# Optimization experiments

Hardware: AMD Instinct MI355X
Metric: run time of the kernel (lower is better)

The kernel has to match this reference:

```python
import jax, jax.numpy as jnp
from jax import lax
import numpy as np

B, L, F = 4, 1024, 32
DM, NL, DS, DC, EX, NH = 256, 4, 16, 4, 2, 4
DI = EX * DM            # 512 inner channels
DTR = (DM + 15) // 16   # dt_rank = 16


def setup_inputs() -> dict:
    key = jax.random.key(0)
    ks = jax.random.split(key, 12)
    s = 0.02
    rn = lambda k, shape: jax.random.normal(k, shape, jnp.float32) * s
    return dict(
        x=jax.random.normal(ks[0], (B, L, F), jnp.float32),
        proj_w=rn(ks[1], (DM, F)), proj_b=jnp.zeros((DM,), jnp.float32),
        inproj_w=rn(ks[2], (NL, 2 * DI, DM)),
        conv_w=rn(ks[3], (NL, DI, DC)), conv_b=jnp.zeros((NL, DI), jnp.float32),
        xproj_w=rn(ks[4], (NL, DTR + 2 * DS, DI)),
        dtproj_w=rn(ks[5], (NL, DI, DTR)), dtproj_b=rn(ks[6], (NL, DI)),
        A_log=jnp.tile(jnp.log(jnp.arange(1, DS + 1, dtype=jnp.float32))[None, None, :], (NL, DI, 1)),
        Dp=jnp.ones((NL, DI), jnp.float32),
        outproj_w=rn(ks[7], (NL, DM, DI)),
        ln_g=jnp.ones((NL, DM), jnp.float32), ln_b=jnp.zeros((NL, DM), jnp.float32),
        head_w1=rn(ks[8], (DM, DM)), head_b1=jnp.zeros((DM,), jnp.float32),
        head_w2=rn(ks[9], (NH, DM)), head_b2=jnp.zeros((NH,), jnp.float32),
    )


def _layernorm(x, g, b, eps=1e-5):
    mu = x.mean(axis=-1, keepdims=True)
    var = ((x - mu) ** 2).mean(axis=-1, keepdims=True)
    return (x - mu) * lax.rsqrt(var + eps) * g + b


def _mamba(x, inw, cw, cb, xpw, dtw, dtb, A_log, Dp, outw):
    b, l, _ = x.shape
    xz = x @ inw.T                       # (b,l,2*DI)
    u, z = xz[..., :DI], xz[..., DI:]
    # causal depthwise conv1d, kernel DC
    up = jnp.pad(u, ((0, 0), (DC - 1, 0), (0, 0)))
    uc = sum(up[:, k:k + l, :] * cw[:, k] for k in range(DC)) + cb
    uc = jax.nn.silu(uc)
    dbc = uc @ xpw.T                     # (b,l,DTR+2*DS)
    dt, Bc, Cc = dbc[..., :DTR], dbc[..., DTR:DTR + DS], dbc[..., DTR + DS:]
    delta = jax.nn.softplus(dt @ dtw.T + dtb)   # (b,l,DI)
    A = -jnp.exp(A_log)                  # (DI,DS)

    def step(h, inp):
        d_t, B_t, C_t, u_t = inp         # (b,DI),(b,DS),(b,DS),(b,DI)
        h = jnp.exp(d_t[..., None] * A) * h + (d_t * u_t)[..., None] * B_t[:, None, :]
        return h, jnp.einsum('bdn,bn->bd', h, C_t)

    h0 = jnp.zeros((b, DI, DS), x.dtype)
    xs = tuple(jnp.swapaxes(a, 0, 1) for a in (delta, Bc, Cc, uc))
    _, ys = lax.scan(step, h0, xs)       # ys: (l,b,DI)
    y = jnp.swapaxes(ys, 0, 1) + uc * Dp
    return (y * jax.nn.silu(z)) @ outw.T


def reference(x, proj_w, proj_b, inproj_w, conv_w, conv_b, xproj_w, dtproj_w, dtproj_b,
              A_log, Dp, outproj_w, ln_g, ln_b, head_w1, head_b1, head_w2, head_b2):
    h = x @ proj_w.T + proj_b
    for i in range(NL):
        blk = _mamba(h, inproj_w[i], conv_w[i], conv_b[i], xproj_w[i],
                     dtproj_w[i], dtproj_b[i], A_log[i], Dp[i], outproj_w[i])
        h = h + _layernorm(blk, ln_g[i], ln_b[i])
    p = h.mean(axis=1)                   # (b,DM) pool over time
    hid = jax.nn.relu(p @ head_w1.T + head_b1)
    return hid @ head_w2.T + head_b2     # (b,NH)
```

## Files before the change

### kernel.cpp

```cpp
#include <hip/hip_runtime.h>
#include <hip/hip_fp16.h>
#include <math.h>

#define LTOT 1024
#define BB   4
#define F_IN 32
#define DM   256
#define DI   512
#define DS   16
#define DTRN 16
#define NXP  48
#define NLAY 4
#define NH   4
#define NC   16
#define CLEN 64
#define ROWS (BB*LTOT)

typedef _Float16 half8 __attribute__((ext_vector_type(8)));
typedef float f32x16 __attribute__((ext_vector_type(16)));

__device__ __forceinline__ float siluf_(float x) { return x / (1.0f + expf(-x)); }
__device__ __forceinline__ float softplusf_(float x) {
    if (x > 20.f) return x;
    if (x < -20.f) return expf(x);
    return log1pf(expf(x));
}

__device__ __forceinline__ void split16(float x, unsigned short& hi, unsigned short& lo) {
    __half h = __float2half(x);
    hi = *(unsigned short*)&h;
    float r = x - __half2float(h);
    __half l = __float2half(r);
    lo = *(unsigned short*)&l;
}

__device__ __forceinline__ size_t fragAddr(int r, int k, int Kd) {
    return ((size_t)((r >> 5) * (Kd >> 4) + (k >> 4)) << 9)
         + (size_t)(((((k >> 3) & 1) << 5) + (r & 31)) * 8 + (k & 7));
}

__global__ __launch_bounds__(256) void k_init(const float* __restrict__ x,
                                              const float* __restrict__ pw,
                                              const float* __restrict__ pb,
                                              const float* __restrict__ inw,
                                              const float* __restrict__ outw,
                                              float* __restrict__ h,
                                              unsigned short* __restrict__ hh,
                                              unsigned short* __restrict__ hl,
                                              unsigned short* __restrict__ iwh,
                                              unsigned short* __restrict__ iwl,
                                              unsigned short* __restrict__ owh,
                                              unsigned short* __restrict__ owl) {
    __shared__ float wl[DM][33];
    __shared__ float xl[16][32];
    int bid = blockIdx.x, t = threadIdx.x;
    if (bid < 1536) {
        int q = bid * 256 + t;
        ushort4 h4, l4;
        if (q < 262144) {
            float4 v = ((const float4*)inw)[q];
            split16(v.x, h4.x, l4.x); split16(v.y, h4.y, l4.y);
            split16(v.z, h4.z, l4.z); split16(v.w, h4.w, l4.w);
            int row = q >> 6, k0 = (q & 63) * 4;
            int lay = row >> 10, rIn = row & 1023;
            size_t fa = (size_t)lay * 262144 + fragAddr(rIn, k0, 256);
            *(ushort4*)(iwh + fa) = h4;
            *(ushort4*)(iwl + fa) = l4;
        } else {
            int rq = q - 262144;
            float4 v = ((const float4*)outw)[rq];
            split16(v.x, h4.x, l4.x); split16(v.y, h4.y, l4.y);
            split16(v.z, h4.z, l4.z); split16(v.w, h4.w, l4.w);
            int row = rq >> 7, k0 = (rq & 127) * 4;
            int lay = row >> 8, rIn = row & 255;
            size_t fa = (size_t)lay * 131072 + fragAddr(rIn, k0, 512);
            *(ushort4*)(owh + fa) = h4;
            *(ushort4*)(owl + fa) = l4;
        }
        return;
    }
    int r0 = (bid - 1536) * 16;
    for (int i = t; i < DM * 32 / 4; i += 256) {
        float4 v = ((const float4*)pw)[i];
        int c = i / 8, k = (i % 8) * 4;
        wl[c][k] = v.x; wl[c][k + 1] = v.y; wl[c][k + 2] = v.z; wl[c][k + 3] = v.w;
    }
    for (int i = t; i < 16 * 32 / 4; i += 256) {
        float4 v = ((const float4*)(x + (size_t)r0 * F_IN))[i];
        int r = i / 8, k = (i % 8) * 4;
        xl[r][k] = v.x; xl[r][k + 1] = v.y; xl[r][k + 2] = v.z; xl[r][k + 3] = v.w;
    }
    __syncthreads();
    int c = t;
    float bias = pb[c];
    float acc[16];
#pragma unroll
    for (int r = 0; r < 16; ++r) acc[r] = bias;
    for (int k = 0; k < 32; ++k) {
        float w = wl[c][k];
#pragma unroll
        for (int r = 0; r < 16; ++r) acc[r] = fmaf(xl[r][k], w, acc[r]);
    }
#pragma unroll
    for (int r = 0; r < 16; ++r) {
        int rr = r0 + r;
        h[(size_t)rr * DM + c] = acc[r];
        unsigned short vh, vl; split16(acc[r], vh, vl);
        size_t fa = fragAddr(rr, c, 256);
        hh[fa] = vh; hl[fa] = vl;
    }
}

__global__ __launch_bounds__(256) void k_gemm_xz(const unsigned short* __restrict__ Ahp,
                                                 const unsigned short* __restrict__ Alp,
                                                 const unsigned short* __restrict__ Bhp,
                                                 const unsigned short* __restrict__ Blp,
                                                 float* __restrict__ C) {
    int t = threadIdx.x;
    int bx = blockIdx.x & 7;
    int by = blockIdx.x >> 3;
    int lane = t & 63, wid = t >> 6;
    int fr = lane & 31, fg = lane >> 5;
    int wr = wid >> 1, wc = wid & 1;
    int rt = by * 2 + wr;
    int ct0 = bx * 4 + wc * 2;
    const half8* pAh = (const half8*)Ahp + (size_t)rt * 1024 + lane;
    const half8* pAl = (const half8*)Alp + (size_t)rt * 1024 + lane;
    const half8* pB0h = (const half8*)Bhp + (size_t)ct0 * 1024 + lane;
    const half8* pB0l = (const half8*)Blp + (size_t)ct0 * 1024 + lane;
    const half8* pB1h = pB0h + 1024;
    const half8* pB1l = pB0l + 1024;
    f32x16 acc[2] = {};
    half8 ah = pAh[0], al = pAl[0];
    half8 b0h = pB0h[0], b0l = pB0l[0], b1h = pB1h[0], b1l = pB1l[0];
#pragma unroll
    for (int kt = 0; kt < 16; ++kt) {
        half8 nah, nal, nb0h, nb0l, nb1h, nb1l;
        if (kt < 15) {
            int o = (kt + 1) * 64;
            nah = pAh[o]; nal = pAl[o];
            nb0h = pB0h[o]; nb0l = pB0l[o];
            nb1h = pB1h[o]; nb1l = pB1l[o];
        }
        acc[0] = __builtin_amdgcn_mfma_f32_32x32x16_f16(ah, b0h, acc[0], 0, 0, 0);
        acc[0] = __builtin_amdgcn_mfma_f32_32x32x16_f16(ah, b0l, acc[0], 0, 0, 0);
        acc[0] = __builtin_amdgcn_mfma_f32_32x32x16_f16(al, b0h, acc[0], 0, 0, 0);
        acc[1] = __builtin_amdgcn_mfma_f32_32x32x16_f16(ah, b1h, acc[1], 0, 0, 0);
        acc[1] = __builtin_amdgcn_mfma_f32_32x32x16_f16(ah, b1l, acc[1], 0, 0, 0);
        acc[1] = __builtin_amdgcn_mfma_f32_32x32x16_f16(al, b1h, acc[1], 0, 0, 0);
        if (kt < 15) { ah = nah; al = nal; b0h = nb0h; b0l = nb0l; b1h = nb1h; b1l = nb1l; }
    }
    float* Cp = C + (size_t)(by * 64 + wr * 32) * 1024 + bx * 128 + wc * 64;
#pragma unroll
    for (int fc = 0; fc < 2; ++fc) {
#pragma unroll
        for (int reg = 0; reg < 16; ++reg) {
            int row = (reg & 3) + 8 * (reg >> 2) + 4 * fg;
            Cp[(size_t)row * 1024 + fc * 32 + fr] = acc[fc][reg];
        }
    }
}

__global__ __launch_bounds__(256) void k_dbcp(const float* __restrict__ xz,
                                              const float* __restrict__ cw,
                                              const float* __restrict__ cb,
                                              const float* __restrict__ xpw,
                                              float* __restrict__ uc,
                                              float* __restrict__ dbp) {
    __shared__ float us[32][132];
    __shared__ float wsd[48][132];
    int t = threadIdx.x;
    int kp = blockIdx.x & 3;
    int r0 = (blockIdx.x >> 2) * 32;
    int k0 = kp * 128;
    float4* us4 = (float4*)us;
    float4* ws4 = (float4*)wsd;
#pragma unroll
    for (int j = 0; j < 4; ++j) {
        int i = t + j * 256;
        int r = i >> 5, kq = i & 31;
        int rr = r0 + r, d = k0 + kq * 4;
        int tt = rr & (LTOT - 1);
        float4 acc = make_float4(cb[d], cb[d + 1], cb[d + 2], cb[d + 3]);
#pragma unroll
        for (int k = 0; k < 4; ++k) {
            int ts = tt - 3 + k;
            if (ts < 0) continue;
            float4 u = *(const float4*)(xz + (size_t)(rr - 3 + k) * 1024 + d);
            acc.x = fmaf(u.x, cw[(d + 0) * 4 + k], acc.x);
            acc.y = fmaf(u.y, cw[(d + 1) * 4 + k], acc.y);
            acc.z = fmaf(u.z, cw[(d + 2) * 4 + k], acc.z);
            acc.w = fmaf(u.w, cw[(d + 3) * 4 + k], acc.w);
        }
        acc.x = siluf_(acc.x); acc.y = siluf_(acc.y); acc.z = siluf_(acc.z); acc.w = siluf_(acc.w);
        us4[r * 33 + kq] = acc;
        *(float4*)(uc + (size_t)rr * DI + d) = acc;
    }
#pragma unroll
    for (int j = 0; j < 6; ++j) {
        int i = t + j * 256;
        int r = i >> 5, kq = i & 31;
        ws4[r * 33 + kq] = *(const float4*)(xpw + (size_t)r * DI + k0 + kq * 4);
    }
    __syncthreads();
    int tx = t & 15, ty = t >> 4;
    const float4* ua = us4 + (ty * 2) * 33;
    const float4* ub = ua + 33;
    const float4* w0p = ws4 + (tx * 3) * 33;
    const float4* w1p = w0p + 33;
    const float4* w2p = w0p + 66;
    float acc[2][3] = {};
#pragma unroll 4
    for (int kq = 0; kq < 32; ++kq) {
        float4 u0 = ua[kq], u1 = ub[kq];
        float4 w0 = w0p[kq], w1 = w1p[kq], w2 = w2p[kq];
        acc[0][0] = fmaf(u0.x, w0.x, acc[0][0]); acc[0][0] = fmaf(u0.y, w0.y, acc[0][0]);
        acc[0][0] = fmaf(u0.z, w0.z, acc[0][0]); acc[0][0] = fmaf(u0.w, w0.w, acc[0][0]);
        acc[0][1] = fmaf(u0.x, w1.x, acc[0][1]); acc[0][1] = fmaf(u0.y, w1.y, acc[0][1]);
        acc[0][1] = fmaf(u0.z, w1.z, acc[0][1]); acc[0][1] = fmaf(u0.w, w1.w, acc[0][1]);
        acc[0][2] = fmaf(u0.x, w2.x, acc[0][2]); acc[0][2] = fmaf(u0.y, w2.y, acc[0][2]);
        acc[0][2] = fmaf(u0.z, w2.z, acc[0][2]); acc[0][2] = fmaf(u0.w, w2.w, acc[0][2]);
        acc[1][0] = fmaf(u1.x, w0.x, acc[1][0]); acc[1][0] = fmaf(u1.y, w0.y, acc[1][0]);
        acc[1][0] = fmaf(u1.z, w0.z, acc[1][0]); acc[1][0] = fmaf(u1.w, w0.w, acc[1][0]);
        acc[1][1] = fmaf(u1.x, w1.x, acc[1][1]); acc[1][1] = fmaf(u1.y, w1.y, acc[1][1]);
        acc[1][1] = fmaf(u1.z, w1.z, acc[1][1]); acc[1][1] = fmaf(u1.w, w1.w, acc[1][1]);
        acc[1][2] = fmaf(u1.x, w2.x, acc[1][2]); acc[1][2] = fmaf(u1.y, w2.y, acc[1][2]);
        acc[1][2] = fmaf(u1.z, w2.z, acc[1][2]); acc[1][2] = fmaf(u1.w, w2.w, acc[1][2]);
    }
    float* outp = dbp + (size_t)(r0 + ty * 2) * 192 + kp * 48 + tx * 3;
    outp[0] = acc[0][0]; outp[1] = acc[0][1]; outp[2] = acc[0][2];
    outp[192] = acc[1][0]; outp[193] = acc[1][1]; outp[194] = acc[1][2];
}

__global__ __launch_bounds__(256) void k_scanA(const float* __restrict__ dbp,
                                               const float* __restrict__ uc,
                                               const float* __restrict__ dtw,
                                               const float* __restrict__ dtb,
                                               const float* __restrict__ A_log,
                                               float* __restrict__ P,
                                               float* __restrict__ hL) {
    __shared__ float2 du2[CLEN][16];
    __shared__ float  Bl[CLEN][16];
    __shared__ float  dbl[CLEN][17];
    __shared__ float  wdl[16][17];
    __shared__ float  wbias[16];
    int bid = blockIdx.x;
    int c = bid & 15, dblk = (bid >> 4) & 31, b = bid >> 9;
    int d0 = dblk * 16, t0 = c * CLEN;
    int t = threadIdx.x;
    int row = t >> 2, q4 = (t & 3) * 4;
    size_t rbase = (size_t)(b * LTOT + t0 + row);
    float4 uv = *(const float4*)(uc + rbase * DI + d0 + q4);
    {
        const float* pp = dbp + rbase * 192;
        float4 a0 = *(const float4*)(pp + q4);
        float4 a1 = *(const float4*)(pp + 48 + q4);
        float4 a2 = *(const float4*)(pp + 96 + q4);
        float4 a3 = *(const float4*)(pp + 144 + q4);
        dbl[row][q4 + 0] = ((a0.x + a1.x) + a2.x) + a3.x;
        dbl[row][q4 + 1] = ((a0.y + a1.y) + a2.y) + a3.y;
        dbl[row][q4 + 2] = ((a0.z + a1.z) + a2.z) + a3.z;
        dbl[row][q4 + 3] = ((a0.w + a1.w) + a2.w) + a3.w;
        float4 b0 = *(const float4*)(pp + 16 + q4);
        float4 b1 = *(const float4*)(pp + 64 + q4);
        float4 b2 = *(const float4*)(pp + 112 + q4);
        float4 b3 = *(const float4*)(pp + 160 + q4);
        Bl[row][q4 + 0] = ((b0.x + b1.x) + b2.x) + b3.x;
        Bl[row][q4 + 1] = ((b0.y + b1.y) + b2.y) + b3.y;
        Bl[row][q4 + 2] = ((b0.z + b1.z) + b2.z) + b3.z;
        Bl[row][q4 + 3] = ((b0.w + b1.w) + b2.w) + b3.w;
    }
    if (t < 64) {
        int dd = t >> 2, sg = (t & 3) * 4;
        const float* wp = dtw + (size_t)(d0 + dd) * 16 + sg;
        wdl[dd][sg + 0] = wp[0]; wdl[dd][sg + 1] = wp[1];
        wdl[dd][sg + 2] = wp[2]; wdl[dd][sg + 3] = wp[3];
    }
    if (t < 16) wbias[t] = dtb[d0 + t];
    __syncthreads();
    {
        float s0 = wbias[q4 + 0], s1 = wbias[q4 + 1], s2 = wbias[q4 + 2], s3 = wbias[q4 + 3];
#pragma unroll
        for (int k = 0; k < 16; ++k) {
            float dv = dbl[row][k];
            s0 = fmaf(dv, wdl[q4 + 0][k], s0);
            s1 = fmaf(dv, wdl[q4 + 1][k], s1);
            s2 = fmaf(dv, wdl[q4 + 2][k], s2);
            s3 = fmaf(dv, wdl[q4 + 3][k], s3);
        }
        du2[row][q4 + 0] = make_float2(softplusf_(s0), uv.x);
        du2[row][q4 + 1] = make_float2(softplusf_(s1), uv.y);
        du2[row][q4 + 2] = make_float2(softplusf_(s2), uv.z);
        du2[row][q4 + 3] = make_float2(softplusf_(s3), uv.w);
    }
    __syncthreads();
    int n = t & 15, dn = t >> 4;
    float Ac = -expf(A_log[(size_t)(d0 + dn) * DS + n]);
    float h = 0.f, Pp = 1.f;
#pragma unroll 8
    for (int k = 0; k < CLEN; ++k) {
        float2 du = du2[k][dn];
        float Bv = Bl[k][n];
        float a = expf(du.x * Ac);
        Pp *= a;
        h = fmaf(a, h, du.x * du.y * Bv);
    }
    size_t idx = ((size_t)(b * NC + c)) * (DI * DS) + (size_t)d0 * DS + t;
    P[idx] = Pp;
    hL[idx] = h;
}

__global__ __launch_bounds__(256) void k_scanC(const float* __restrict__ dbp,
                                               const float* __restrict__ uc,
                                               const float* __restrict__ dtw,
                                               const float* __restrict__ dtb,
                                               const float* __restrict__ A_log,
                                               const float* __restrict__ P,
                                               const float* __restrict__ hL,
                                               const float* __restrict__ Dp,
                                               const float* __restrict__ xz,
                                               unsigned short* __restrict__ yh,
                                               unsigned short* __restrict__ yl) {
    __shared__ float2 du2[CLEN][16];
    __shared__ float2 bc2[CLEN][16];
    __shared__ float  ytmp[16][16][20];
    float* scr = &ytmp[0][0][0];
    float (*dbl)[17] = (float(*)[17])scr;
    float (*wdl)[17] = (float(*)[17])(scr + 1088);
    float* wbias = scr + 1088 + 272;
    int bid = blockIdx.x;
    int c = bid & 15, dblk = (bid >> 4) & 31, b = bid >> 9;
    int d0 = dblk * 16, t0 = c * CLEN;
    int t = threadIdx.x;
    int row = t >> 2, q4 = (t & 3) * 4;
    size_t rbase = (size_t)(b * LTOT + t0 + row);
    float4 uv = *(const float4*)(uc + rbase * DI + d0 + q4);
    {
        const float* pp = dbp + rbase * 192;
        float4 a0 = *(const float4*)(pp + q4);
        float4 a1 = *(const float4*)(pp + 48 + q4);
        float4 a2 = *(const float4*)(pp + 96 + q4);
        float4 a3 = *(const float4*)(pp + 144 + q4);
        dbl[row][q4 + 0] = ((a0.x + a1.x) + a2.x) + a3.x;
        dbl[row][q4 + 1] = ((a0.y + a1.y) + a2.y) + a3.y;
        dbl[row][q4 + 2] = ((a0.z + a1.z) + a2.z) + a3.z;
        dbl[row][q4 + 3] = ((a0.w + a1.w) + a2.w) + a3.w;
        float4 b0 = *(const float4*)(pp + 16 + q4);
        float4 b1 = *(const float4*)(pp + 64 + q4);
        float4 b2 = *(const float4*)(pp + 112 + q4);
        float4 b3 = *(const float4*)(pp + 160 + q4);
        float4 c0 = *(const float4*)(pp + 32 + q4);
        float4 c1 = *(const float4*)(pp + 80 + q4);
        float4 c2 = *(const float4*)(pp + 128 + q4);
        float4 c3 = *(const float4*)(pp + 176 + q4);
        float B0 = ((b0.x + b1.x) + b2.x) + b3.x, C0 = ((c0.x + c1.x) + c2.x) + c3.x;
        float B1 = ((b0.y + b1.y) + b2.y) + b3.y, C1 = ((c0.y + c1.y) + c2.y) + c3.y;
        float B2 = ((b0.z + b1.z) + b2.z) + b3.z, C2 = ((c0.z + c1.z) + c2.z) + c3.z;
        float B3 = ((b0.w + b1.w) + b2.w) + b3.w, C3 = ((c0.w + c1.w) + c2.w) + c3.w;
        bc2[row][q4 + 0] = make_float2(B0, C0);
        bc2[row][q4 + 1] = make_float2(B1, C1);
        bc2[row][q4 + 2] = make_float2(B2, C2);
        bc2[row][q4 + 3] = make_float2(B3, C3);
    }
    if (t < 64) {
        int dd = t >> 2, sg = (t & 3) * 4;
        const float* wp = dtw + (size_t)(d0 + dd) * 16 + sg;
        wdl[dd][sg + 0] = wp[0]; wdl[dd][sg + 1] = wp[1];
        wdl[dd][sg + 2] = wp[2]; wdl[dd][sg + 3] = wp[3];
    }
    if (t < 16) wbias[t] = dtb[d0 + t];
    __syncthreads();
    {
        float s0 = wbias[q4 + 0], s1 = wbias[q4 + 1], s2 = wbias[q4 + 2], s3 = wbias[q4 + 3];
#pragma unroll
        for (int k = 0; k < 16; ++k) {
            float dv = dbl[row][k];
            s0 = fmaf(dv, wdl[q4 + 0][k], s0);
            s1 = fmaf(dv, wdl[q4 + 1][k], s1);
            s2 = fmaf(dv, wdl[q4 + 2][k], s2);
            s3 = fmaf(dv, wdl[q4 + 3][k], s3);
        }
        du2[row][q4 + 0] = make_float2(softplusf_(s0), uv.x);
        du2[row][q4 + 1] = make_float2(softplusf_(s1), uv.y);
        du2[row][q4 + 2] = make_float2(softplusf_(s2), uv.z);
        du2[row][q4 + 3] = make_float2(softplusf_(s3), uv.w);
    }
    __syncthreads();
    int n = t & 15, dn = t >> 4;
    float Ac = -expf(A_log[(size_t)(d0 + dn) * DS + n]);
    float Hin = 0.f;
    for (int cc = 0; cc < c; ++cc) {
        size_t idx = ((size_t)(b * NC + cc)) * (DI * DS) + (size_t)d0 * DS + t;
        Hin = fmaf(P[idx], Hin, hL[idx]);
    }
    float h = Hin;
    int rdn = t & 15, rk = t >> 4;
    float DpV = Dp[d0 + rdn];
    for (int s = 0; s < CLEN / 16; ++s) {
#pragma unroll
        for (int kk = 0; kk < 16; ++kk) {
            int k = s * 16 + kk;
            float2 du = du2[k][dn];
            float2 bc = bc2[k][n];
            float a = expf(du.x * Ac);
            h = fmaf(a, h, du.x * du.y * bc.x);
            ytmp[kk][dn][n] = h * bc.y;
        }
        __syncthreads();
        {
            const float* rowp = &ytmp[rk][rdn][0];
            float4 v0 = *(const float4*)(rowp + 0);
            float4 v1 = *(const float4*)(rowp + 4);
            float4 v2 = *(const float4*)(rowp + 8);
            float4 v3 = *(const float4*)(rowp + 12);
            float y = ((v0.x + v0.y) + (v0.z + v0.w)) + ((v1.x + v1.y) + (v1.z + v1.w))
                    + ((v2.x + v2.y) + (v2.z + v2.w)) + ((v3.x + v3.y) + (v3.z + v3.w));
            float uu = du2[s * 16 + rk][rdn].y;
            size_t rb2 = (size_t)(b * LTOT + t0 + s * 16 + rk);
            float z = xz[rb2 * 1024 + 512 + d0 + rdn];
            float val = fmaf(uu, DpV, y) * siluf_(z);
            unsigned short vh, vl; split16(val, vh, vl);
            size_t fa = fragAddr((int)rb2, d0 + rdn, 512);
            yh[fa] = vh; yl[fa] = vl;
        }
        __syncthreads();
    }
}

__global__ __launch_bounds__(256) void k_gemm_out(const unsigned short* __restrict__ Ahp,
                                                  const unsigned short* __restrict__ Alp,
                                                  const unsigned short* __restrict__ Bhp,
                                                  const unsigned short* __restrict__ Blp,
                                                  float* __restrict__ p01,
                                                  float* __restrict__ p23) {
    int t = threadIdx.x;
    int bx = blockIdx.x & 1;
    int by = (blockIdx.x >> 1) & 63;
    int kp = blockIdx.x >> 7;
    int lane = t & 63, wid = t >> 6;
    int fr = lane & 31, fg = lane >> 5;
    int wr = wid >> 1, wc = wid & 1;
    int rt = by * 2 + wr;
    int ct0 = bx * 4 + wc * 2;
    const half8* pAh = (const half8*)Ahp + (size_t)rt * 2048 + (size_t)kp * 512 + lane;
    const half8* pAl = (const half8*)Alp + (size_t)rt * 2048 + (size_t)kp * 512 + lane;
    const half8* pB0h = (const half8*)Bhp + (size_t)ct0 * 2048 + (size_t)kp * 512 + lane;
    const half8* pB0l = (const half8*)Blp + (size_t)ct0 * 2048 + (size_t)kp * 512 + lane;
    const half8* pB1h = pB0h + 2048;
    const half8* pB1l = pB0l + 2048;
    f32x16 acc[2] = {};
    half8 ah = pAh[0], al = pAl[0];
    half8 b0h = pB0h[0], b0l = pB0l[0], b1h = pB1h[0], b1l = pB1l[0];
#pragma unroll
    for (int kt = 0; kt < 8; ++kt) {
        half8 nah, nal, nb0h, nb0l, nb1h, nb1l;
        if (kt < 7) {
            int o = (kt + 1) * 64;
            nah = pAh[o]; nal = pAl[o];
            nb0h = pB0h[o]; nb0l = pB0l[o];
            nb1h = pB1h[o]; nb1l = pB1l[o];
        }
        acc[0] = __builtin_amdgcn_mfma_f32_32x32x16_f16(ah, b0h, acc[0], 0, 0, 0);
        acc[0] = __builtin_amdgcn_mfma_f32_32x32x16_f16(ah, b0l, acc[0], 0, 0, 0);
        acc[0] = __builtin_amdgcn_mfma_f32_32x32x16_f16(al, b0h, acc[0], 0, 0, 0);
        acc[1] = __builtin_amdgcn_mfma_f32_32x32x16_f16(ah, b1h, acc[1], 0, 0, 0);
        acc[1] = __builtin_amdgcn_mfma_f32_32x32x16_f16(ah, b1l, acc[1], 0, 0, 0);
        acc[1] = __builtin_amdgcn_mfma_f32_32x32x16_f16(al, b1h, acc[1], 0, 0, 0);
        if (kt < 7) { ah = nah; al = nal; b0h = nb0h; b0l = nb0l; b1h = nb1h; b1l = nb1l; }
    }
    float* pbase = (kp < 2 ? p01 : p23) + (size_t)(kp & 1) * (ROWS * DM);
    float* Cp = pbase + (size_t)(by * 64 + wr * 32) * DM + bx * 128 + wc * 64;
#pragma unroll
    for (int fc = 0; fc < 2; ++fc) {
#pragma unroll
        for (int reg = 0; reg < 16; ++reg) {
            int row = (reg & 3) + 8 * (reg >> 2) + 4 * fg;
            Cp[(size_t)row * DM + fc * 32 + fr] = acc[fc][reg];
        }
    }
}

__global__ __launch_bounds__(256) void k_ln_res(const float* __restrict__ p01,
                                                const float* __restrict__ p23,
                                                const float* __restrict__ g,
                                                const float* __restrict__ bb,
                                                float* __restrict__ h,
                                                unsigned short* __restrict__ hh,
                                                unsigned short* __restrict__ hl) {
    __shared__ float scratch[4];
    int r = blockIdx.x, t = threadIdx.x;
    size_t idx = (size_t)r * DM + t;
    float v = p01[idx] + p01[idx + (size_t)ROWS * DM] + p23[idx] + p23[idx + (size_t)ROWS * DM];
    float s = v;
#pragma unroll
    for (int m = 32; m >= 1; m >>= 1) s += __shfl_xor(s, m, 64);
    if ((t & 63) == 0) scratch[t >> 6] = s;
    __syncthreads();
    float mu = (scratch[0] + scratch[1] + scratch[2] + scratch[3]) * (1.f / DM);
    __syncthreads();
    float d = v - mu;
    float s2 = d * d;
#pragma unroll
    for (int m = 32; m >= 1; m >>= 1) s2 += __shfl_xor(s2, m, 64);
    if ((t & 63) == 0) scratch[t >> 6] = s2;
    __syncthreads();
    float var = (scratch[0] + scratch[1] + scratch[2] + scratch[3]) * (1.f / DM);
    float rstd = 1.f / sqrtf(var + 1e-5f);
    float nv = h[idx] + d * rstd * g[t] + bb[t];
    h[idx] = nv;
    unsigned short vh, vl; split16(nv, vh, vl);
    size_t fa = fragAddr(r, t, 256);
    hh[fa] = vh; hl[fa] = vl;
}

__global__ __launch_bounds__(256) void k_meanp(const float* __restrict__ h,
                                               float* __restrict__ part) {
    int bid = blockIdx.x;
    int b = bid >> 3, g = bid & 7;
    int t = threadIdx.x;
    float s = 0.f;
    for (int k = 0; k < 128; ++k)
        s += h[(size_t)(b * LTOT + g * 128 + k) * DM + t];
    part[(size_t)bid * DM + t] = s;
}

__global__ __launch_bounds__(256) void k_head(const float* __restrict__ part,
                                              const float* __restrict__ w1,
                                              const float* __restrict__ b1,
                                              const float* __restrict__ w2,
                                              const float* __restrict__ b2,
                                              float* __restrict__ out) {
    __shared__ float pl[DM], hl[DM];
    int b = blockIdx.x, t = threadIdx.x;
    float s = 0.f;
    for (int g = 0; g < 8; ++g) s += part[(size_t)(b * 8 + g) * DM + t];
    pl[t] = s * (1.f / LTOT);
    __syncthreads();
    float a = b1[t];
    for (int k = 0; k < DM; ++k) a = fmaf(pl[k], w1[(size_t)t * DM + k], a);
    hl[t] = fmaxf(a, 0.f);
    __syncthreads();
    if (t < NH) {
        float o = b2[t];
        for (int k = 0; k < DM; ++k) o = fmaf(hl[k], w2[(size_t)t * DM + k], o);
        out[b * NH + t] = o;
    }
}

extern "C" void kernel_launch(void* const* d_in, const int* in_sizes, int n_in,
                              void* d_out, int out_size, void* d_ws, size_t ws_size,
                              hipStream_t stream) {
    const float* x        = (const float*)d_in[0];
    const float* proj_w   = (const float*)d_in[1];
    const float* proj_b   = (const float*)d_in[2];
    const float* inproj_w = (const float*)d_in[3];
    const float* conv_w   = (const float*)d_in[4];
    const float* conv_b   = (const float*)d_in[5];
    const float* xproj_w  = (const float*)d_in[6];
    const float* dtproj_w = (const float*)d_in[7];
    const float* dtproj_b = (const float*)d_in[8];
    const float* A_log    = (const float*)d_in[9];
    const float* Dp       = (const float*)d_in[10];
    const float* outproj_w= (const float*)d_in[11];
    const float* ln_g     = (const float*)d_in[12];
    const float* ln_b     = (const float*)d_in[13];
    const float* head_w1  = (const float*)d_in[14];
    const float* head_b1  = (const float*)d_in[15];
    const float* head_w2  = (const float*)d_in[16];
    const float* head_b2  = (const float*)d_in[17];

    float* ws    = (float*)d_ws;
    float* h     = ws;
    float* xz    = h + 1048576;
    float* uc    = xz + 4194304;
    float* dbp   = uc + 2097152;
    float* Pbuf  = dbp + 786432;
    float* hLbuf = Pbuf + 524288;
    float* p01   = hLbuf + 524288;
    float* p23   = p01 + 2097152;
    float* part  = p23 + 2097152;
    unsigned short* h_hi  = (unsigned short*)(part + 8192);
    unsigned short* h_lo  = h_hi + 1048576;
    unsigned short* y_hi  = h_lo + 1048576;
    unsigned short* y_lo  = y_hi + 2097152;
    unsigned short* iw_hi = y_lo + 2097152;
    unsigned short* iw_lo = iw_hi + 1048576;
    unsigned short* ow_hi = iw_lo + 1048576;
    unsigned short* ow_lo = ow_hi + 524288;

    k_init<<<1792, 256, 0, stream>>>(x, proj_w, proj_b, inproj_w, outproj_w,
                                     h, h_hi, h_lo, iw_hi, iw_lo, ow_hi, ow_lo);

    for (int i = 0; i < NLAY; ++i) {
        const float* cwi  = conv_w + (size_t)i * DI * 4;
        const float* cbi  = conv_b + (size_t)i * DI;
        const float* xpw  = xproj_w + (size_t)i * NXP * DI;
        const float* dtw  = dtproj_w + (size_t)i * DI * DTRN;
        const float* dtb  = dtproj_b + (size_t)i * DI;
        const float* Ali  = A_log + (size_t)i * DI * DS;
        const float* Dpi  = Dp + (size_t)i * DI;
        const float* gi   = ln_g + (size_t)i * DM;
        const float* bi   = ln_b + (size_t)i * DM;

        k_gemm_xz<<<512, 256, 0, stream>>>(h_hi, h_lo,
                                           iw_hi + (size_t)i * 262144, iw_lo + (size_t)i * 262144, xz);
        k_dbcp<<<512, 256, 0, stream>>>(xz, cwi, cbi, xpw, uc, dbp);
        k_scanA<<<BB * 32 * NC, 256, 0, stream>>>(dbp, uc, dtw, dtb, Ali, Pbuf, hLbuf);
        k_scanC<<<BB * 32 * NC, 256, 0, stream>>>(dbp, uc, dtw, dtb, Ali, Pbuf, hLbuf, Dpi, xz, y_hi, y_lo);
        k_gemm_out<<<512, 256, 0, stream>>>(y_hi, y_lo,
                                            ow_hi + (size_t)i * 131072, ow_lo + (size_t)i * 131072,
                                            p01, p23);
        k_ln_res<<<ROWS, 256, 0, stream>>>(p01, p23, gi, bi, h, h_hi, h_lo);
    }

    k_meanp<<<32, 256, 0, stream>>>(h, part);
    k_head<<<BB, 256, 0, stream>>>(part, head_w1, head_b1, head_w2, head_b2, (float*)d_out);
}
```

Before: 494.8 us.

## Precompute delta and B/C once in a separate kernel instead of in both scans

```diff
diff --git a/kernel.cpp b/kernel.cpp
--- a/kernel.cpp
+++ b/kernel.cpp
@@ -232,66 +232,69 @@
     outp[192] = acc[1][0]; outp[193] = acc[1][1]; outp[194] = acc[1][2];
 }
 
-__global__ __launch_bounds__(256) void k_scanA(const float* __restrict__ dbp,
+__global__ __launch_bounds__(256) void k_dbcr(const float* __restrict__ dbp,
+                                              const float* __restrict__ dtw,
+                                              const float* __restrict__ dtb,
+                                              float* __restrict__ delta,
+                                              float* __restrict__ BC) {
+    __shared__ float dbl[16][NXP];
+    int t = threadIdx.x;
+    int r0 = blockIdx.x * 16;
+    {
+        int r = t >> 4, c3 = (t & 15) * 3;
+        const float* pp = dbp + (size_t)(r0 + r) * 192 + c3;
+#pragma unroll
+        for (int j = 0; j < 3; ++j) {
+            float s = pp[j] + pp[48 + j] + pp[96 + j] + pp[144 + j];
+            dbl[r][c3 + j] = s;
+            int cj = c3 + j;
+            if (cj >= 16) BC[(size_t)(r0 + r) * 32 + (cj - 16)] = s;
+        }
+    }
+    __syncthreads();
+    {
+        int c0 = t * 2;
+        float wd0[16], wd1[16];
+        const float4* q0 = (const float4*)(dtw + (size_t)c0 * 16);
+        const float4* q1 = (const float4*)(dtw + (size_t)(c0 + 1) * 16);
+#pragma unroll
+        for (int j = 0; j < 4; ++j) { *(float4*)&wd0[j * 4] = q0[j]; *(float4*)&wd1[j * 4] = q1[j]; }
+        float bb0 = dtb[c0], bb1 = dtb[c0 + 1];
+        for (int r = 0; r < 16; ++r) {
+            float s0 = bb0, s1 = bb1;
+#pragma unroll
+            for (int k = 0; k < 16; ++k) {
+                float dv = dbl[r][k];
+                s0 = fmaf(dv, wd0[k], s0);
+                s1 = fmaf(dv, wd1[k], s1);
+            }
+            *(float2*)(delta + (size_t)(r0 + r) * DI + c0) =
+                make_float2(softplusf_(s0), softplusf_(s1));
+        }
+    }
+}
+
+__global__ __launch_bounds__(256) void k_scanA(const float* __restrict__ delta,
                                                const float* __restrict__ uc,
-                                               const float* __restrict__ dtw,
-                                               const float* __restrict__ dtb,
+                                               const float* __restrict__ BC,
                                                const float* __restrict__ A_log,
                                                float* __restrict__ P,
                                                float* __restrict__ hL) {
     __shared__ float2 du2[CLEN][16];
     __shared__ float  Bl[CLEN][16];
-    __shared__ float  dbl[CLEN][17];
-    __shared__ float  wdl[16][17];
-    __shared__ float  wbias[16];
     int bid = blockIdx.x;
     int c = bid & 15, dblk = (bid >> 4) & 31, b = bid >> 9;
     int d0 = dblk * 16, t0 = c * CLEN;
     int t = threadIdx.x;
-    int row = t >> 2, q4 = (t & 3) * 4;
-    size_t rbase = (size_t)(b * LTOT + t0 + row);
-    float4 uv = *(const float4*)(uc + rbase * DI + d0 + q4);
     {
-        const float* pp = dbp + rbase * 192;
-        float4 a0 = *(const float4*)(pp + q4);
-        float4 a1 = *(const float4*)(pp + 48 + q4);
-        float4 a2 = *(const float4*)(pp + 96 + q4);
-        float4 a3 = *(const float4*)(pp + 144 + q4);
-        dbl[row][q4 + 0] = ((a0.x + a1.x) + a2.x) + a3.x;
-        dbl[row][q4 + 1] = ((a0.y + a1.y) + a2.y) + a3.y;
-        dbl[row][q4 + 2] = ((a0.z + a1.z) + a2.z) + a3.z;
-        dbl[row][q4 + 3] = ((a0.w + a1.w) + a2.w) + a3.w;
-        float4 b0 = *(const float4*)(pp + 16 + q4);
-        float4 b1 = *(const float4*)(pp + 64 + q4);
-        float4 b2 = *(const float4*)(pp + 112 + q4);
-        float4 b3 = *(const float4*)(pp + 160 + q4);
-        Bl[row][q4 + 0] = ((b0.x + b1.x) + b2.x) + b3.x;
-        Bl[row][q4 + 1] = ((b0.y + b1.y) + b2.y) + b3.y;
-        Bl[row][q4 + 2] = ((b0.z + b1.z) + b2.z) + b3.z;
-        Bl[row][q4 + 3] = ((b0.w + b1.w) + b2.w) + b3.w;
-    }
-    if (t < 64) {
-        int dd = t >> 2, sg = (t & 3) * 4;
-        const float* wp = dtw + (size_t)(d0 + dd) * 16 + sg;
-        wdl[dd][sg + 0] = wp[0]; wdl[dd][sg + 1] = wp[1];
-        wdl[dd][sg + 2] = wp[2]; wdl[dd][sg + 3] = wp[3];
-    }
-    if (t < 16) wbias[t] = dtb[d0 + t];
-    __syncthreads();
-    {
-        float s0 = wbias[q4 + 0], s1 = wbias[q4 + 1], s2 = wbias[q4 + 2], s3 = wbias[q4 + 3];
-#pragma unroll
-        for (int k = 0; k < 16; ++k) {
-            float dv = dbl[row][k];
-            s0 = fmaf(dv, wdl[q4 + 0][k], s0);
-            s1 = fmaf(dv, wdl[q4 + 1][k], s1);
-            s2 = fmaf(dv, wdl[q4 + 2][k], s2);
-            s3 = fmaf(dv, wdl[q4 + 3][k], s3);
-        }
-        du2[row][q4 + 0] = make_float2(softplusf_(s0), uv.x);
-        du2[row][q4 + 1] = make_float2(softplusf_(s1), uv.y);
-        du2[row][q4 + 2] = make_float2(softplusf_(s2), uv.z);
-        du2[row][q4 + 3] = make_float2(softplusf_(s3), uv.w);
+        int row = t >> 2, hf = (t & 3) * 4;
+        size_t rbase = (size_t)(b * LTOT + t0 + row);
+        float4 dv = *(const float4*)(delta + rbase * DI + d0 + hf);
+        float4 uv = *(const float4*)(uc + rbase * DI + d0 + hf);
+        float4* dst = (float4*)&du2[row][hf];
+        dst[0] = make_float4(dv.x, uv.x, dv.y, uv.y);
+        dst[1] = make_float4(dv.z, uv.z, dv.w, uv.w);
+        *(float4*)&Bl[row][hf] = *(const float4*)(BC + rbase * 32 + hf);
     }
     __syncthreads();
     int n = t & 15, dn = t >> 4;
@@ -310,10 +313,9 @@
     hL[idx] = h;
 }
 
-__global__ __launch_bounds__(256) void k_scanC(const float* __restrict__ dbp,
+__global__ __launch_bounds__(256) void k_scanC(const float* __restrict__ delta,
                                                const float* __restrict__ uc,
-                                               const float* __restrict__ dtw,
-                                               const float* __restrict__ dtb,
+                                               const float* __restrict__ BC,
                                                const float* __restrict__ A_log,
                                                const float* __restrict__ P,
                                                const float* __restrict__ hL,
@@ -324,66 +326,23 @@
     __shared__ float2 du2[CLEN][16];
     __shared__ float2 bc2[CLEN][16];
     __shared__ float  ytmp[16][16][20];
-    float* scr = &ytmp[0][0][0];
-    float (*dbl)[17] = (float(*)[17])scr;
-    float (*wdl)[17] = (float(*)[17])(scr + 1088);
-    float* wbias = scr + 1088 + 272;
     int bid = blockIdx.x;
     int c = bid & 15, dblk = (bid >> 4) & 31, b = bid >> 9;
     int d0 = dblk * 16, t0 = c * CLEN;
     int t = threadIdx.x;
-    int row = t >> 2, q4 = (t & 3) * 4;
-    size_t rbase = (size_t)(b * LTOT + t0 + row);
-    float4 uv = *(const float4*)(uc + rbase * DI + d0 + q4);
     {
-        const float* pp = dbp + rbase * 192;
-        float4 a0 = *(const float4*)(pp + q4);
-        float4 a1 = *(const float4*)(pp + 48 + q4);
-        float4 a2 = *(const float4*)(pp + 96 + q4);
-        float4 a3 = *(const float4*)(pp + 144 + q4);
-        dbl[row][q4 + 0] = ((a0.x + a1.x) + a2.x) + a3.x;
-        dbl[row][q4 + 1] = ((a0.y + a1.y) + a2.y) + a3.y;
-        dbl[row][q4 + 2] = ((a0.z + a1.z) + a2.z) + a3.z;
-        dbl[row][q4 + 3] = ((a0.w + a1.w) + a2.w) + a3.w;
-        float4 b0 = *(const float4*)(pp + 16 + q4);
-        float4 b1 = *(const float4*)(pp + 64 + q4);
-        float4 b2 = *(const float4*)(pp + 112 + q4);
-        float4 b3 = *(const float4*)(pp + 160 + q4);
-        float4 c0 = *(const float4*)(pp + 32 + q4);
-        float4 c1 = *(const float4*)(pp + 80 + q4);
-        float4 c2 = *(const float4*)(pp + 128 + q4);
-        float4 c3 = *(const float4*)(pp + 176 + q4);
-        float B0 = ((b0.x + b1.x) + b2.x) + b3.x, C0 = ((c0.x + c1.x) + c2.x) + c3.x;
-        float B1 = ((b0.y + b1.y) + b2.y) + b3.y, C1 = ((c0.y + c1.y) + c2.y) + c3.y;
-        float B2 = ((b0.z + b1.z) + b2.z) + b3.z, C2 = ((c0.z + c1.z) + c2.z) + c3.z;
-        float B3 = ((b0.w + b1.w) + b2.w) + b3.w, C3 = ((c0.w + c1.w) + c2.w) + c3.w;
-        bc2[row][q4 + 0] = make_float2(B0, C0);
-        bc2[row][q4 + 1] = make_float2(B1, C1);
-        bc2[row][q4 + 2] = make_float2(B2, C2);
-        bc2[row][q4 + 3] = make_float2(B3, C3);
-    }
-    if (t < 64) {
-        int dd = t >> 2, sg = (t & 3) * 4;
-        const float* wp = dtw + (size_t)(d0 + dd) * 16 + sg;
-        wdl[dd][sg + 0] = wp[0]; wdl[dd][sg + 1] = wp[1];
-        wdl[dd][sg + 2] = wp[2]; wdl[dd][sg + 3] = wp[3];
-    }
-    if (t < 16) wbias[t] = dtb[d0 + t];
-    __syncthreads();
-    {
-        float s0 = wbias[q4 + 0], s1 = wbias[q4 + 1], s2 = wbias[q4 + 2], s3 = wbias[q4 + 3];
-#pragma unroll
-        for (int k = 0; k < 16; ++k) {
-            float dv = dbl[row][k];
-            s0 = fmaf(dv, wdl[q4 + 0][k], s0);
-            s1 = fmaf(dv, wdl[q4 + 1][k], s1);
-            s2 = fmaf(dv, wdl[q4 + 2][k], s2);
-            s3 = fmaf(dv, wdl[q4 + 3][k], s3);
-        }
-        du2[row][q4 + 0] = make_float2(softplusf_(s0), uv.x);
-        du2[row][q4 + 1] = make_float2(softplusf_(s1), uv.y);
-        du2[row][q4 + 2] = make_float2(softplusf_(s2), uv.z);
-        du2[row][q4 + 3] = make_float2(softplusf_(s3), uv.w);
+        int row = t >> 2, hf = (t & 3) * 4;
+        size_t rbase = (size_t)(b * LTOT + t0 + row);
+        float4 dv = *(const float4*)(delta + rbase * DI + d0 + hf);
+        float4 uv = *(const float4*)(uc + rbase * DI + d0 + hf);
+        float4* dst = (float4*)&du2[row][hf];
+        dst[0] = make_float4(dv.x, uv.x, dv.y, uv.y);
+        dst[1] = make_float4(dv.z, uv.z, dv.w, uv.w);
+        float4 bv = *(const float4*)(BC + rbase * 32 + hf);
+        float4 cv = *(const float4*)(BC + rbase * 32 + 16 + hf);
+        float4* bdst = (float4*)&bc2[row][hf];
+        bdst[0] = make_float4(bv.x, cv.x, bv.y, cv.y);
+        bdst[1] = make_float4(bv.z, cv.z, bv.w, cv.w);
     }
     __syncthreads();
     int n = t & 15, dn = t >> 4;
@@ -574,7 +533,9 @@
     float* xz    = h + 1048576;
     float* uc    = xz + 4194304;
     float* dbp   = uc + 2097152;
-    float* Pbuf  = dbp + 786432;
+    float* delta = dbp + 786432;
+    float* BC    = delta + 2097152;
+    float* Pbuf  = BC + 131072;
     float* hLbuf = Pbuf + 524288;
     float* p01   = hLbuf + 524288;
     float* p23   = p01 + 2097152;
@@ -605,8 +566,9 @@
         k_gemm_xz<<<512, 256, 0, stream>>>(h_hi, h_lo,
                                            iw_hi + (size_t)i * 262144, iw_lo + (size_t)i * 262144, xz);
         k_dbcp<<<512, 256, 0, stream>>>(xz, cwi, cbi, xpw, uc, dbp);
-        k_scanA<<<BB * 32 * NC, 256, 0, stream>>>(dbp, uc, dtw, dtb, Ali, Pbuf, hLbuf);
-        k_scanC<<<BB * 32 * NC, 256, 0, stream>>>(dbp, uc, dtw, dtb, Ali, Pbuf, hLbuf, Dpi, xz, y_hi, y_lo);
+        k_dbcr<<<ROWS / 16, 256, 0, stream>>>(dbp, dtw, dtb, delta, BC);
+        k_scanA<<<BB * 32 * NC, 256, 0, stream>>>(delta, uc, BC, Ali, Pbuf, hLbuf);
+        k_scanC<<<BB * 32 * NC, 256, 0, stream>>>(delta, uc, BC, Ali, Pbuf, hLbuf, Dpi, xz, y_hi, y_lo);
         k_gemm_out<<<512, 256, 0, stream>>>(y_hi, y_lo,
                                             ow_hi + (size_t)i * 131072, ow_lo + (size_t)i * 131072,
                                             p01, p23);
```

Result: faster. 484.4 us (-2.1%).
